# Optimization experiments

Hardware: AMD Instinct MI355X
Metric: run time of the kernel (lower is better)

The kernel has to match this reference:

```python
import jax, jax.numpy as jnp
import numpy as np
from jax import lax

K_SQ = 8  # scaling-and-squaring steps (GridExp default)


def lrelu(x):
    return jnp.where(x >= 0, x, 0.2 * x)


def conv(x, w, b, stride=1):
    y = lax.conv_general_dilated(x, w, (stride,) * 3, 'SAME',
                                 dimension_numbers=('NCDHW', 'OIDHW', 'NCDHW'))
    return y + b[None, :, None, None, None]


def convt(x, w, b):
    y = lax.conv_transpose(x, w, (2, 2, 2), 'SAME',
                           dimension_numbers=('NCDHW', 'OIDHW', 'NCDHW'))
    return y + b[None, :, None, None, None]


def identity_grid(shape):
    rng = [jnp.arange(s, dtype=jnp.float32) for s in shape]
    return jnp.stack(jnp.meshgrid(*rng, indexing='ij'), axis=-1)


def pull_one(img, grid, extrapolate):
    # img (C, X, Y, Z); grid (..., 3) in voxel coordinates; trilinear sampling
    X, Y, Z = img.shape[1:]
    g0f = jnp.floor(grid)
    w = grid - g0f
    g0 = g0f.astype(jnp.int32)
    flat = img.reshape(img.shape[0], -1)
    out = jnp.zeros(img.shape[:1] + grid.shape[:-1], img.dtype)
    for dx in (0, 1):
        for dy in (0, 1):
            for dz in (0, 1):
                ix = jnp.clip(g0[..., 0] + dx, 0, X - 1)
                iy = jnp.clip(g0[..., 1] + dy, 0, Y - 1)
                iz = jnp.clip(g0[..., 2] + dz, 0, Z - 1)
                idx = (ix * Y + iy) * Z + iz
                val = jnp.take(flat, idx.reshape(-1), axis=1).reshape(out.shape)
                wgt = ((w[..., 0] if dx else 1 - w[..., 0]) *
                       (w[..., 1] if dy else 1 - w[..., 1]) *
                       (w[..., 2] if dz else 1 - w[..., 2]))
                out = out + wgt[None] * val
    if not extrapolate:  # zero outside the field of view (GridPull extrapolate=False)
        inb = ((grid[..., 0] >= 0) & (grid[..., 0] <= X - 1) &
               (grid[..., 1] >= 0) & (grid[..., 1] <= Y - 1) &
               (grid[..., 2] >= 0) & (grid[..., 2] <= Z - 1))
        out = out * inb[None]
    return out


pull_batch = jax.vmap(pull_one, in_axes=(0, 0, None))


def resize_field(field, out_shape, value_scale):
    # field (B, X, Y, Z, D) channel-last; trilinear resize (align-centers), scale values
    in_shape = field.shape[1:-1]
    coords = identity_grid(out_shape)
    scale = jnp.array([(i - 1) / (o - 1) for i, o in zip(in_shape, out_shape)], jnp.float32)
    coords = coords * scale
    f = jnp.moveaxis(field, -1, 1)
    cb = jnp.broadcast_to(coords, (field.shape[0],) + coords.shape)
    out = pull_batch(f, cb, True)
    return jnp.moveaxis(out, 1, -1) * value_scale


def affine_basis_cso():
    # CSO in 3D: 3 translations + 3 rotations + 1 isotropic zoom -> 7 params
    B = np.zeros((7, 4, 4), np.float32)
    for i in range(3):
        B[i, i, 3] = 1.0
    for k, (i, j) in enumerate([(0, 1), (0, 2), (1, 2)]):
        B[3 + k, i, j] = 1.0
        B[3 + k, j, i] = -1.0
    for i in range(3):
        B[6, i, i] = 1.0
    return jnp.asarray(B)


def forward_core(source, target, cnn_w, cnn_b, enc_w, enc_b, up_w, up_b, dec_w, dec_b, fin_w, fin_b):
    x = jnp.concatenate([source, target], axis=1)  # (B, 2, X, Y, Z)
    # ---- affine head CNN: 4 strided convs + head conv + global reduction -> (B, 7)
    h = x
    for i in range(4):
        h = lrelu(conv(h, cnn_w[i], cnn_b[i], stride=2))
    h = conv(h, cnn_w[4], cnn_b[4])
    aff_prm = h.mean(axis=(2, 3, 4))
    # ---- UNet velocity head -> (B, X, Y, Z, 3)
    skips = [x]
    h = x
    for i in range(4):
        h = lrelu(conv(h, enc_w[i], enc_b[i], stride=2))
        skips.append(h)
    for i in range(4):
        h = lrelu(convt(h, up_w[i], up_b[i]))
        h = jnp.concatenate([h, skips[3 - i]], axis=1)
        h = lrelu(conv(h, dec_w[i], dec_b[i]))
    vel = jnp.moveaxis(conv(h, fin_w, fin_b), 1, -1)
    shape = vel.shape[1:-1]
    small = tuple(s // 2 for s in shape)
    # ---- exp(): downsample velocity (displacement: values scaled by 0.5)
    v_small = resize_field(vel, small, 0.5)
    idg = identity_grid(small)
    d = v_small / (2.0 ** K_SQ)
    for _ in range(K_SQ):  # scaling and squaring: d <- d + d o (id + d)
        d = d + jnp.moveaxis(pull_batch(jnp.moveaxis(d, -1, 1), idg[None] + d, True), 1, -1)
    grid = resize_field(idg[None] + d, shape, 2.0)  # grid: coords scaled by 2
    # ---- affine exponential, re-centered composition
    basis = affine_basis_cso()
    A = jax.vmap(lambda p: jax.scipy.linalg.expm(jnp.einsum('k,kij->ij', p, basis)))(aff_prm)
    shift = jnp.eye(4, dtype=jnp.float32).at[:3, 3].set(-jnp.asarray(shape, jnp.float32) / 2)
    A = jnp.linalg.solve(shift[None], A @ shift[None])  # inv(shift) @ A @ shift
    lin, off = A[:, :3, :3], A[:, :3, 3]
    grid = jnp.einsum('bij,bxyzj->bxyzi', lin, grid) + off[:, None, None, None, :]
    # ---- warp source
    deformed = pull_batch(source, grid, False)
    return deformed, vel, aff_prm


def setup_inputs() -> dict:
    key = jax.random.key(0)
    ks = iter(jax.random.split(key, 48))

    def p(shape):
        return jax.random.normal(next(ks), shape, jnp.float32) * 0.05

    d = {}
    d['source'] = jax.random.normal(next(ks), (1, 1, 96, 96, 96), jnp.float32)
    d['target'] = jax.random.normal(next(ks), (1, 1, 96, 96, 96), jnp.float32)
    for i, (o, c) in enumerate([(16, 2), (32, 16), (32, 32), (32, 32), (7, 32)]):
        d[f'cnn_w{i}'] = p((o, c, 3, 3, 3)); d[f'cnn_b{i}'] = p((o,))
    for i, (o, c) in enumerate([(16, 2), (32, 16), (32, 32), (32, 32)]):
        d[f'enc_w{i}'] = p((o, c, 3, 3, 3)); d[f'enc_b{i}'] = p((o,))
    for i, (o, c) in enumerate([(32, 32), (32, 32), (32, 32), (16, 32)]):
        d[f'up_w{i}'] = p((o, c, 3, 3, 3)); d[f'up_b{i}'] = p((o,))
    for i, (o, c) in enumerate([(32, 64), (32, 64), (32, 48), (16, 18)]):
        d[f'dec_w{i}'] = p((o, c, 3, 3, 3)); d[f'dec_b{i}'] = p((o,))
    d['fin_w'] = p((3, 16, 3, 3, 3)); d['fin_b'] = p((3,))
    return d


def reference(source, target,
              cnn_w0, cnn_b0, cnn_w1, cnn_b1, cnn_w2, cnn_b2, cnn_w3, cnn_b3, cnn_w4, cnn_b4,
              enc_w0, enc_b0, enc_w1, enc_b1, enc_w2, enc_b2, enc_w3, enc_b3,
              up_w0, up_b0, up_w1, up_b1, up_w2, up_b2, up_w3, up_b3,
              dec_w0, dec_b0, dec_w1, dec_b1, dec_w2, dec_b2, dec_w3, dec_b3,
              fin_w, fin_b):
    return forward_core(
        source, target,
        [cnn_w0, cnn_w1, cnn_w2, cnn_w3, cnn_w4], [cnn_b0, cnn_b1, cnn_b2, cnn_b3, cnn_b4],
        [enc_w0, enc_w1, enc_w2, enc_w3], [enc_b0, enc_b1, enc_b2, enc_b3],
        [up_w0, up_w1, up_w2, up_w3], [up_b0, up_b1, up_b2, up_b3],
        [dec_w0, dec_w1, dec_w2, dec_w3], [dec_b0, dec_b1, dec_b2, dec_b3],
        fin_w, fin_b)
```

## Files before the change

### kernel.cpp

```cpp
#include <hip/hip_runtime.h>

#define N96 884736
#define N48 110592
#define N24 13824
#define N12 1728
#define N6  216

typedef __attribute__((ext_vector_type(4))) short short4v;
typedef __attribute__((ext_vector_type(8))) short short8v;
typedef __attribute__((ext_vector_type(4))) float f32x4;

static __device__ __forceinline__ float lrelu_f(float x){ return x >= 0.f ? x : 0.2f*x; }
static __device__ __forceinline__ int clampi(int v,int lo,int hi){ return v<lo?lo:(v>hi?hi:v); }

static __device__ __forceinline__ short f2bf(float x){
    unsigned u = __builtin_bit_cast(unsigned, x);
    unsigned r = (u + 0x7FFFu + ((u >> 16) & 1u)) >> 16;
    return (short)r;
}

template<int OCPB, int S, bool RELU>
static __device__ __forceinline__ void conv_body(
    const float* __restrict__ in1, int C1,
    const float* __restrict__ in2, int C2,
    const float* __restrict__ w, const float* __restrict__ b,
    float* __restrict__ out, int ID, int OD,
    long out_cstride, int out_vmul, int t, int oc0)
{
    int i2 = t % OD; int r = t / OD; int i1 = r % OD; int i0 = r / OD;

    float acc[OCPB];
    #pragma unroll
    for (int j=0; j<OCPB; ++j) acc[j] = b[oc0+j];

    int zz[3], yy[3], xx[3]; bool zv[3], yv[3], xv[3];
    #pragma unroll
    for (int k=0; k<3; ++k){
        int a0 = (S==2) ? (2*i0+k) : (i0+k-1);
        int a1 = (S==2) ? (2*i1+k) : (i1+k-1);
        int a2 = (S==2) ? (2*i2+k) : (i2+k-1);
        zz[k]=a0; zv[k]=(a0>=0)&&(a0<ID);
        yy[k]=a1; yv[k]=(a1>=0)&&(a1<ID);
        xx[k]=a2; xv[k]=(a2>=0)&&(a2<ID);
    }
    const int C = C1 + C2;
    const int ID2 = ID*ID;
    const long ID3 = (long)ID2*ID;

    for (int s=0; s<2; ++s){
        const float* ip = s ? in2 : in1;
        int Cs  = s ? C2 : C1;
        int icb = s ? C1 : 0;
        if (Cs == 0) continue;
        for (int ic=0; ic<Cs; ++ic){
            const float* ipb = ip + (long)ic*ID3;
            float v[27];
            #pragma unroll
            for (int kd=0; kd<3; ++kd)
            #pragma unroll
            for (int kh=0; kh<3; ++kh)
            #pragma unroll
            for (int kw=0; kw<3; ++kw){
                bool ok = zv[kd] && yv[kh] && xv[kw];
                v[kd*9+kh*3+kw] = ok ? ipb[(long)zz[kd]*ID2 + yy[kh]*ID + xx[kw]] : 0.f;
            }
            const float* wbase = w + ((long)oc0*C + (icb+ic))*27;
            #pragma unroll
            for (int j=0; j<OCPB; ++j){
                const float* wo = wbase + (long)j*C*27;
                float sacc = 0.f;
                #pragma unroll
                for (int k=0; k<27; ++k) sacc += wo[k]*v[k];
                acc[j] += sacc;
            }
        }
    }
    #pragma unroll
    for (int j=0; j<OCPB; ++j){
        float o = RELU ? lrelu_f(acc[j]) : acc[j];
        out[(long)(oc0+j)*out_cstride + (long)t*out_vmul] = o;
    }
}

template<int OCPB, int S, bool RELU>
__global__ void conv3d_k(const float* __restrict__ in1, int C1,
                         const float* __restrict__ in2, int C2,
                         const float* __restrict__ w, const float* __restrict__ b,
                         float* __restrict__ out, int ID, int OD,
                         long out_cstride, int out_vmul)
{
    int nvox = OD*OD*OD;
    int t = blockIdx.x*blockDim.x + threadIdx.x;
    if (t >= nvox) return;
    conv_body<OCPB,S,RELU>(in1,C1,in2,C2,w,b,out,ID,OD,out_cstride,out_vmul,t,blockIdx.y*OCPB);
}

template<int OCPB, int S, bool RELU>
__global__ void conv3d_dual_k(const float* __restrict__ in1A, const float* __restrict__ in2A,
                              const float* __restrict__ in1B, const float* __restrict__ in2B,
                              int C1, int C2,
                              const float* __restrict__ wA, const float* __restrict__ bA,
                              const float* __restrict__ wB, const float* __restrict__ bB,
                              float* __restrict__ outA, float* __restrict__ outB,
                              int ID, int OD)
{
    int nvox = OD*OD*OD;
    int t = blockIdx.x*blockDim.x + threadIdx.x;
    if (t >= nvox) return;
    long nv = nvox;
    if (blockIdx.z == 0)
        conv_body<OCPB,S,RELU>(in1A,C1,in2A,C2,wA,bA,outA,ID,OD,nv,1,t,blockIdx.y*OCPB);
    else
        conv_body<OCPB,S,RELU>(in1B,C1,in2B,C2,wB,bB,outB,ID,OD,nv,1,t,blockIdx.y*OCPB);
}

__global__ void e0cl16_k(const float* __restrict__ e0, short* __restrict__ cl){
    int t = blockIdx.x*blockDim.x + threadIdx.x;
    if (t >= N48) return;
    short8v v0, v1;
    #pragma unroll
    for (int c=0;c<8;++c){ v0[c] = f2bf(e0[(long)c*N48 + t]); v1[c] = f2bf(e0[(long)(8+c)*N48 + t]); }
    *(short8v*)(cl + (long)t*16)     = v0;
    *(short8v*)(cl + (long)t*16 + 8) = v1;
}

__global__ __launch_bounds__(256, 2)
void conv_s2mfma_k(const short* __restrict__ cl,
                   const short* __restrict__ pack,
                   const float* __restrict__ b,
                   float* __restrict__ out)
{
    const short8v zero8 = {0,0,0,0,0,0,0,0};
    int lane = threadIdx.x & 63;
    int nb = gridDim.x;
    int bid = blockIdx.x;
    int sb = (bid & 7)*(nb >> 3) + (bid >> 3);
    int wid = sb*4 + (threadIdx.x >> 6);
    int ot = wid & 1;
    int s  = wid >> 1;
    int l15 = lane & 15, g = lane >> 4;
    int vL = s*16 + l15;
    int xL = vL % 24; int rL = vL/24; int yL = rL % 24; int zL = rL/24;
    const bool gok = (g < 2);

    float bias = b[ot*16 + l15];
    f32x4 acc = {bias,bias,bias,bias};

    #pragma unroll
    for (int kz=0; kz<3; ++kz){
        int iz = 2*zL + kz; bool okz = (iz < 48);
        int izc = okz ? iz : 0;
        #pragma unroll
        for (int ky=0; ky<3; ++ky){
            int iy = 2*yL + ky; bool oky = (iy < 48);
            int iyc = oky ? iy : 0;
            #pragma unroll
            for (int kx=0; kx<3; ++kx){
                int ix = 2*xL + kx; bool okx = (ix < 48);
                int ixc = okx ? ix : 0;
                bool ok = okz && oky && okx && gok;
                long base = (((long)izc*48 + iyc)*48 + ixc)*16 + (gok ? 8*g : 0);
                short8v a = *(const short8v*)(cl + base);
                if (!ok) a = zero8;
                int kidx = kz*9 + ky*3 + kx;
                short8v wfr = *(const short8v*)(pack + (((long)ot*27 + kidx)*64 + lane)*8);
                acc = __builtin_amdgcn_mfma_f32_16x16x32_bf16(a, wfr, acc, 0, 0, 0);
            }
        }
    }

    int oc = ot*16 + l15;
    #pragma unroll
    for (int reg=0; reg<4; ++reg){
        int m = 4*g + reg;
        out[(long)oc*N24 + s*16 + m] = lrelu_f(acc[reg]);
    }
}

__global__ void e3cl_k(const float* __restrict__ e3, short* __restrict__ cl){
    int t = blockIdx.x*blockDim.x + threadIdx.x;
    if (t >= N6) return;
    #pragma unroll
    for (int grp=0; grp<4; ++grp){
        short8v v;
        #pragma unroll
        for (int c=0;c<8;++c) v[c] = f2bf(e3[(long)(8*grp+c)*N6 + t]);
        *(short8v*)(cl + (long)t*32 + 8*grp) = v;
    }
}

__global__ void fill_e0_k(const float* __restrict__ e0, short* __restrict__ cl){
    int t = blockIdx.x*blockDim.x + threadIdx.x;
    if (t >= N48) return;
    short8v v0, v1;
    #pragma unroll
    for (int c=0;c<8;++c)  v0[c] = f2bf(e0[(long)c*N48 + t]);
    #pragma unroll
    for (int c=0;c<8;++c)  v1[c] = f2bf(e0[(long)(8+c)*N48 + t]);
    *(short8v*)(cl + (long)t*48 + 32) = v0;
    *(short8v*)(cl + (long)t*48 + 40) = v1;
}

template<int NV>
__global__ void fill_skip32_k(const float* __restrict__ e, short* __restrict__ cl){
    int t = blockIdx.x*blockDim.x + threadIdx.x;
    if (t >= NV) return;
    #pragma unroll
    for (int grp=0; grp<4; ++grp){
        short8v v;
        #pragma unroll
        for (int c=0;c<8;++c) v[c] = f2bf(e[(long)(8*grp+c)*NV + t]);
        *(short8v*)(cl + (long)t*64 + 32 + 8*grp) = v;
    }
}

static __device__ __forceinline__ void pack_std_d(const float* __restrict__ w, short* __restrict__ pack,
                                                  int t, int CREAL, int OCREAL){
    int kidx = t >> 6, lane = t & 63;
    int oc = lane & 15, g = lane >> 4;
    short8v f;
    #pragma unroll
    for (int j=0;j<8;++j){
        int ic = 8*g + j;
        float val = (oc < OCREAL && ic < CREAL) ? w[((long)oc*CREAL + ic)*27 + kidx] : 0.f;
        f[j] = f2bf(val);
    }
    *(short8v*)(pack + (long)t*8) = f;
}
static __device__ __forceinline__ void pack_2x2_d(const float* __restrict__ w, short* __restrict__ pack,
                                                  int t, int C){
    int lane = t & 63;
    int r = t >> 6;
    int kidx = r % 27;
    int kt = (r/27) & 1;
    int ot = r/54;
    int oc = ot*16 + (lane & 15), g = lane >> 4;
    short8v f;
    #pragma unroll
    for (int j=0;j<8;++j){
        int ic = kt*32 + 8*g + j;
        float val = (ic < C) ? w[((long)oc*C + ic)*27 + kidx] : 0.f;
        f[j] = f2bf(val);
    }
    *(short8v*)(pack + (long)t*8) = f;
}
static __device__ __forceinline__ void pack_up_d(const float* __restrict__ w, short* __restrict__ pack, int t){
    int lane = t & 63;
    int r = t >> 6;
    int kidx = r % 27;
    int ot = r/27;
    int oc = ot*16 + (lane & 15), g = lane >> 4;
    short8v f;
    #pragma unroll
    for (int j=0;j<8;++j){
        int ic = 8*g + j;
        f[j] = f2bf(w[((long)oc*32 + ic)*27 + kidx]);
    }
    *(short8v*)(pack + (long)t*8) = f;
}
static __device__ __forceinline__ void pack_s2_d(const float* __restrict__ w, short* __restrict__ pack, int t){
    int lane = t & 63;
    int r = t >> 6;
    int kidx = r % 27;
    int ot = r/27;
    int oc = ot*16 + (lane & 15), g = lane >> 4;
    short8v f;
    #pragma unroll
    for (int j=0;j<8;++j){
        int ic = 8*g + j;
        float val = (ic < 16) ? w[((long)oc*16 + ic)*27 + kidx] : 0.f;
        f[j] = f2bf(val);
    }
    *(short8v*)(pack + (long)t*8) = f;
}

__global__ void pack_all_k(const float* __restrict__ dw3, const float* __restrict__ fw,
                           const float* __restrict__ uw3,
                           const float* __restrict__ dw2, const float* __restrict__ dw1,
                           const float* __restrict__ dw0,
                           const float* __restrict__ uw2, const float* __restrict__ uw1,
                           const float* __restrict__ uw0,
                           const float* __restrict__ ew1,
                           short* __restrict__ PK3, short* __restrict__ PKF, short* __restrict__ PKU,
                           short* __restrict__ PK2, short* __restrict__ PK1, short* __restrict__ PK0,
                           short* __restrict__ PKU2, short* __restrict__ PKU1, short* __restrict__ PKU0,
                           short* __restrict__ PKE1)
{
    int t = blockIdx.x*blockDim.x + threadIdx.x;
    const int S1 = 27*64;
    const int S4 = 4*27*64;
    const int S2 = 2*27*64;
    if (t < S1){ pack_std_d(dw3, PK3, t, 18, 16); return; } t -= S1;
    if (t < S1){ pack_std_d(fw,  PKF, t, 16,  3); return; } t -= S1;
    if (t < S1){ pack_std_d(uw3, PKU, t, 32, 16); return; } t -= S1;
    if (t < S4){ pack_2x2_d(dw2, PK2, t, 48); return; } t -= S4;
    if (t < S4){ pack_2x2_d(dw1, PK1, t, 64); return; } t -= S4;
    if (t < S4){ pack_2x2_d(dw0, PK0, t, 64); return; } t -= S4;
    if (t < S2){ pack_up_d(uw2, PKU2, t); return; } t -= S2;
    if (t < S2){ pack_up_d(uw1, PKU1, t); return; } t -= S2;
    if (t < S2){ pack_up_d(uw0, PKU0, t); return; } t -= S2;
    if (t < S2){ pack_s2_d(ew1, PKE1, t); return; }
}

template<int CSTR, int OCREAL, bool RELU, int OMODE>
__global__ __launch_bounds__(256, 4)
void conv_mfma2_k(const short* __restrict__ cl,
                  const short* __restrict__ pack,
                  const float* __restrict__ b,
                  void* __restrict__ outp)
{
    const int D2 = 96*96;
    const short8v zero8 = {0,0,0,0,0,0,0,0};
    __shared__ short lwfr[27*64*8];
    for (int idx = threadIdx.x; idx < 27*64; idx += 256)
        *(short8v*)(lwfr + (long)idx*8) = *(const short8v*)(pack + (long)idx*8);
    __syncthreads();

    int lane = threadIdx.x & 63;
    int nb = gridDim.x;
    int bid = blockIdx.x;
    int sb = (bid & 7)*(nb >> 3) + (bid >> 3);
    int wid = sb*4 + (threadIdx.x >> 6);
    int l15 = lane & 15, g = lane >> 4;
    int xh = wid & 1;
    int rem = wid >> 1;
    int y = rem % 96;
    int z = (rem / 96)*2;
    int x0b = xh*48;
    const bool gok = (8*g < CSTR);
    const int go = gok ? 8*g : 0;

    float bias = (l15 < OCREAL) ? b[l15] : 0.f;
    f32x4 acc[2][3];
    #pragma unroll
    for (int o=0;o<2;++o)
    #pragma unroll
    for (int i=0;i<3;++i) acc[o][i] = (f32x4){bias,bias,bias,bias};

    #pragma unroll
    for (int dzr=-1; dzr<=2; ++dzr){
        int zz = z + dzr;
        bool okz = (zz>=0) && (zz<96);
        int zc = okz ? zz : z;
        #pragma unroll
        for (int dy=-1; dy<=1; ++dy){
            int yy = y+dy;
            bool okrow = okz && (yy>=0) && (yy<96);
            int yc = (yy>=0 && yy<96) ? yy : y;
            long rowb = (long)zc*D2 + (long)yc*96;
            #pragma unroll
            for (int dx=-1; dx<=1; ++dx){
                short8v a[3];
                #pragma unroll
                for (int i=0;i<3;++i){
                    int x = x0b + 16*i + l15 + dx;
                    bool okx = (x>=0) && (x<96);
                    int xc = okx ? x : (x0b + 16*i + l15);
                    a[i] = *(const short8v*)(cl + (rowb + xc)*CSTR + go);
                    bool oka = okrow && okx && gok;
                    if (!oka) a[i] = zero8;
                }
                if (dzr >= -1 && dzr <= 1){
                    int kidx = (dzr+1)*9 + (dy+1)*3 + (dx+1);
                    short8v wfr = *(const short8v*)(lwfr + ((long)kidx*64 + lane)*8);
                    #pragma unroll
                    for (int i=0;i<3;++i)
                        acc[0][i] = __builtin_amdgcn_mfma_f32_16x16x32_bf16(a[i], wfr, acc[0][i], 0, 0, 0);
                }
                if (dzr >= 0 && dzr <= 2){
                    int kidx = (dzr)*9 + (dy+1)*3 + (dx+1);
                    short8v wfr = *(const short8v*)(lwfr + ((long)kidx*64 + lane)*8);
                    #pragma unroll
                    for (int i=0;i<3;++i)
                        acc[1][i] = __builtin_amdgcn_mfma_f32_16x16x32_bf16(a[i], wfr, acc[1][i], 0, 0, 0);
                }
            }
        }
    }

    #pragma unroll
    for (int o=0;o<2;++o){
        long vrow = (long)(z+o)*D2 + (long)y*96 + x0b;
        if (OMODE == 0){
            short* op = (short*)outp;
            #pragma unroll
            for (int i=0;i<3;++i)
            #pragma unroll
            for (int reg=0; reg<4; ++reg){
                int mr = 4*g + reg;
                float v = RELU ? lrelu_f(acc[o][i][reg]) : acc[o][i][reg];
                op[(vrow + 16*i + mr)*16 + l15] = f2bf(v);
            }
        } else {
            float* op = (float*)outp;
            if (l15 < 3){
                #pragma unroll
                for (int i=0;i<3;++i)
                #pragma unroll
                for (int reg=0; reg<4; ++reg){
                    int mr = 4*g + reg;
                    op[(vrow + 16*i + mr)*3 + l15] = acc[o][i][reg];
                }
            }
        }
    }
}

__global__ __launch_bounds__(256, 2)
void conv_mfma48_k(const short* __restrict__ cl,
                   const short* __restrict__ pack,
                   const float* __restrict__ b,
                   short* __restrict__ out)
{
    const int D2 = 48*48;
    const short8v zero8 = {0,0,0,0,0,0,0,0};
    int lane = threadIdx.x & 63;
    int nb = gridDim.x;
    int bid = blockIdx.x;
    int sb = (bid & 7)*(nb >> 3) + (bid >> 3);
    int wid = sb*4 + (threadIdx.x >> 6);
    int l15 = lane & 15, g = lane >> 4;
    int y = wid % 48, z = wid / 48;
    const bool g1ok = (g < 2);
    const int go1 = g1ok ? (32 + 8*g) : 0;

    float bias0 = b[l15];
    float bias1 = b[16 + l15];
    f32x4 acc[2][3];
    #pragma unroll
    for (int i=0;i<3;++i){ acc[0][i] = (f32x4){bias0,bias0,bias0,bias0};
                           acc[1][i] = (f32x4){bias1,bias1,bias1,bias1}; }

    #pragma unroll
    for (int dz=-1; dz<=1; ++dz){
        int zz = z+dz;
        bool okz = (zz>=0) && (zz<48);
        int zc = okz ? zz : z;
        #pragma unroll
        for (int dy=-1; dy<=1; ++dy){
            int yy = y+dy;
            bool okzy = okz && (yy>=0) && (yy<48);
            int yc = (yy>=0 && yy<48) ? yy : y;
            long rowb = (long)zc*D2 + (long)yc*48;
            #pragma unroll
            for (int dx=-1; dx<=1; ++dx){
                int kidx = (dz+1)*9 + (dy+1)*3 + (dx+1);
                short8v a0[3], a1[3];
                #pragma unroll
                for (int i=0;i<3;++i){
                    int x = 16*i + l15 + dx;
                    bool okx = (x>=0) && (x<48);
                    int xc = okx ? x : (16*i + l15);
                    bool ok = okzy && okx;
                    long base = (rowb + xc)*48;
                    a0[i] = *(const short8v*)(cl + base + 8*g);
                    a1[i] = *(const short8v*)(cl + base + go1);
                    if (!ok) a0[i] = zero8;
                    if (!(ok && g1ok)) a1[i] = zero8;
                }
                #pragma unroll
                for (int ot=0; ot<2; ++ot){
                    short8v wfr0 = *(const short8v*)(pack + (((long)(ot*2+0)*27 + kidx)*64 + lane)*8);
                    short8v wfr1 = *(const short8v*)(pack + (((long)(ot*2+1)*27 + kidx)*64 + lane)*8);
                    #pragma unroll
                    for (int i=0;i<3;++i){
                        acc[ot][i] = __builtin_amdgcn_mfma_f32_16x16x32_bf16(a0[i], wfr0, acc[ot][i], 0, 0, 0);
                        acc[ot][i] = __builtin_amdgcn_mfma_f32_16x16x32_bf16(a1[i], wfr1, acc[ot][i], 0, 0, 0);
                    }
                }
            }
        }
    }

    long vrow = (long)z*D2 + (long)y*48;
    #pragma unroll
    for (int ot=0; ot<2; ++ot)
    #pragma unroll
    for (int i=0;i<3;++i)
    #pragma unroll
    for (int reg=0; reg<4; ++reg){
        int mr = 4*g + reg;
        out[(vrow + 16*i + mr)*32 + ot*16 + l15] = f2bf(lrelu_f(acc[ot][i][reg]));
    }
}

template<int D>
__global__ __launch_bounds__(256, 2)
void conv_mfmaD_k(const short* __restrict__ cl,
                  const short* __restrict__ pack,
                  const float* __restrict__ b,
                  short* __restrict__ out)
{
    const short8v zero8 = {0,0,0,0,0,0,0,0};
    int lane = threadIdx.x & 63;
    int nb = gridDim.x;
    int bid = blockIdx.x;
    int sb = ((nb & 7) == 0) ? ((bid & 7)*(nb >> 3) + (bid >> 3)) : bid;
    int wid = sb*4 + (threadIdx.x >> 6);
    int ot = wid & 1;
    int s  = wid >> 1;
    int l15 = lane & 15, g = lane >> 4;
    int vL = s*16 + l15;
    int xL = vL % D; int rL = vL/D; int yL = rL % D; int zL = rL/D;

    float bias = b[ot*16 + l15];
    f32x4 acc = {bias,bias,bias,bias};

    #pragma unroll
    for (int dz=-1; dz<=1; ++dz){
        int iz = zL+dz; bool okz = (iz>=0)&&(iz<D); int izc = okz?iz:zL;
        #pragma unroll
        for (int dy=-1; dy<=1; ++dy){
            int iy = yL+dy; bool oky = (iy>=0)&&(iy<D); int iyc = oky?iy:yL;
            #pragma unroll
            for (int dx=-1; dx<=1; ++dx){
                int ix = xL+dx; bool okx = (ix>=0)&&(ix<D); int ixc = okx?ix:xL;
                bool ok = okz && oky && okx;
                long base = (((long)izc*D + iyc)*D + ixc)*64;
                int kidx = (dz+1)*9 + (dy+1)*3 + (dx+1);
                #pragma unroll
                for (int kt=0; kt<2; ++kt){
                    short8v wfr = *(const short8v*)(pack + (((long)(ot*2+kt)*27 + kidx)*64 + lane)*8);
                    short8v a = *(const short8v*)(cl + base + kt*32 + 8*g);
                    if (!ok) a = zero8;
                    acc = __builtin_amdgcn_mfma_f32_16x16x32_bf16(a, wfr, acc, 0, 0, 0);
                }
            }
        }
    }

    #pragma unroll
    for (int reg=0; reg<4; ++reg){
        int m = 4*g + reg;
        out[(long)(s*16 + m)*32 + ot*16 + l15] = f2bf(lrelu_f(acc[reg]));
    }
}

template<int IDI, int NST, int OSTR>
__global__ __launch_bounds__(256, 2)
void convt_mfmaup_k(const short* __restrict__ cl,
                    const short* __restrict__ pack,
                    const float* __restrict__ b,
                    short* __restrict__ o)
{
    const int D2i = IDI*IDI;
    const int OD = 2*IDI;
    const long D2o = (long)OD*OD;
    int lane = threadIdx.x & 63;
    int nb = gridDim.x;
    int bid = blockIdx.x;
    int sb = ((nb & 7) == 0) ? ((bid & 7)*(nb >> 3) + (bid >> 3)) : bid;
    int wid = sb*4 + (threadIdx.x >> 6);
    int px = wid & 1;
    int row = wid >> 1;
    int y = row % OD, z = row / OD;
    int l15 = lane & 15, g = lane >> 4;
    int pz = z & 1, py = y & 1, hz = z >> 1, hy = y >> 1;

    float bias0 = b[l15], bias1 = b[16 + l15];
    f32x4 acc[2][NST];
    #pragma unroll
    for (int i=0;i<NST;++i){ acc[0][i] = (f32x4){bias0,bias0,bias0,bias0};
                             acc[1][i] = (f32x4){bias1,bias1,bias1,bias1}; }

    int k0s[2], izs[2], nz=0;
    if (pz){ k0s[0]=1; izs[0]=hz; nz=1; }
    else { if (hz>=1){ k0s[nz]=0; izs[nz]=hz-1; ++nz; } k0s[nz]=2; izs[nz]=hz; ++nz; }
    int k1s[2], iys[2], ny=0;
    if (py){ k1s[0]=1; iys[0]=hy; ny=1; }
    else { if (hy>=1){ k1s[ny]=0; iys[ny]=hy-1; ++ny; } k1s[ny]=2; iys[ny]=hy; ++ny; }

    for (int a=0;a<nz;++a)
    for (int c=0;c<ny;++c){
        long rowb = (long)izs[a]*D2i + (long)iys[c]*IDI;
        int kbase = k0s[a]*9 + k1s[c]*3;
        int nqx = px?1:2;
        for (int qx=0; qx<nqx; ++qx){
            int k2 = px ? 1 : 2*qx;
            int xoff = px ? 0 : (qx-1);
            short8v av[NST];
            #pragma unroll
            for (int i=0;i<NST;++i){
                int ix = 16*i + l15 + xoff;
                av[i] = (short8v){0,0,0,0,0,0,0,0};
                if (ix >= 0 && ix < IDI) av[i] = *(const short8v*)(cl + ((rowb + ix)*32 + 8*g));
            }
            #pragma unroll
            for (int ot=0; ot<2; ++ot){
                short8v wfr = *(const short8v*)(pack + (((long)ot*27 + kbase + k2)*64 + lane)*8);
                #pragma unroll
                for (int i=0;i<NST;++i)
                    acc[ot][i] = __builtin_amdgcn_mfma_f32_16x16x32_bf16(av[i], wfr, acc[ot][i], 0, 0, 0);
            }
        }
    }

    #pragma unroll
    for (int ot=0; ot<2; ++ot)
    #pragma unroll
    for (int i=0;i<NST;++i)
    #pragma unroll
    for (int reg=0; reg<4; ++reg){
        int m = 16*i + 4*g + reg;
        if (m < IDI){
            long vox = (long)z*D2o + (long)y*OD + (2*m + px);
            o[vox*OSTR + ot*16 + l15] = f2bf(lrelu_f(acc[ot][i][reg]));
        }
    }
}

__global__ __launch_bounds__(256, 2)
void convt_mfma96_k(const short* __restrict__ cl,
                    const short* __restrict__ pack,
                    const float* __restrict__ b,
                    const float* __restrict__ src,
                    const float* __restrict__ tgt,
                    short* __restrict__ o)
{
    const int D2i = 48*48;
    const long D2o = 96*96;
    int lane = threadIdx.x & 63;
    int nb = gridDim.x;
    int bid = blockIdx.x;
    int sb = (bid & 7)*(nb >> 3) + (bid >> 3);
    int wid = sb*4 + (threadIdx.x >> 6);
    int px = wid & 1;
    int row = wid >> 1;
    int y = row % 96, z = row / 96;
    int l15 = lane & 15, g = lane >> 4;
    int pz = z & 1, py = y & 1, hz = z >> 1, hy = y >> 1;

    float bias = b[l15];
    f32x4 acc[3];
    #pragma unroll
    for (int i=0;i<3;++i) acc[i] = (f32x4){bias,bias,bias,bias};

    int k0s[2], izs[2], nz=0;
    if (pz){ k0s[0]=1; izs[0]=hz; nz=1; }
    else { if (hz>=1){ k0s[nz]=0; izs[nz]=hz-1; ++nz; } k0s[nz]=2; izs[nz]=hz; ++nz; }
    int k1s[2], iys[2], ny=0;
    if (py){ k1s[0]=1; iys[0]=hy; ny=1; }
    else { if (hy>=1){ k1s[ny]=0; iys[ny]=hy-1; ++ny; } k1s[ny]=2; iys[ny]=hy; ++ny; }

    for (int a=0;a<nz;++a)
    for (int c=0;c<ny;++c){
        long rowb = (long)izs[a]*D2i + (long)iys[c]*48;
        int kbase = k0s[a]*9 + k1s[c]*3;
        int nqx = px?1:2;
        for (int qx=0; qx<nqx; ++qx){
            int k2 = px ? 1 : 2*qx;
            int xoff = px ? 0 : (qx-1);
            short8v wfr = *(const short8v*)(pack + ((long)(kbase+k2)*64 + lane)*8);
            #pragma unroll
            for (int i=0;i<3;++i){
                int ix = 16*i + l15 + xoff;
                short8v av = {0,0,0,0,0,0,0,0};
                if (ix >= 0) av = *(const short8v*)(cl + ((rowb + ix)*32 + 8*g));
                acc[i] = __builtin_amdgcn_mfma_f32_16x16x32_bf16(av, wfr, acc[i], 0, 0, 0);
            }
        }
    }

    #pragma unroll
    for (int i=0;i<3;++i)
    #pragma unroll
    for (int reg=0; reg<4; ++reg){
        int m = 16*i + 4*g + reg;
        long vox = (long)z*D2o + (long)y*96 + (2*m + px);
        o[vox*24 + l15] = f2bf(lrelu_f(acc[i][reg]));
        if (l15 == 0)      o[vox*24 + 16] = f2bf(src[vox]);
        else if (l15 == 1) o[vox*24 + 17] = f2bf(tgt[vox]);
        else if (l15 < 8)  o[vox*24 + 16 + l15] = 0;
    }
}

static __device__ void mat4mul(const double* A, const double* B, double* C){
    for (int i=0;i<4;++i) for (int j=0;j<4;++j){
        double s=0; for (int k=0;k<4;++k) s += A[i*4+k]*B[k*4+j];
        C[i*4+j]=s;
    }
}

__global__ void affine_k(const float* __restrict__ c4, float* __restrict__ aff_out, float* __restrict__ mats){
    __shared__ float p[7];
    int t = threadIdx.x;
    if (t < 7){
        float s = 0.f;
        for (int i=0;i<N6;++i) s += c4[t*N6 + i];
        p[t] = s / (float)N6;
        aff_out[t] = p[t];
    }
    __syncthreads();
    if (t == 0){
        double M[16];
        for (int i=0;i<16;++i) M[i]=0.0;
        M[0*4+3]=p[0]; M[1*4+3]=p[1]; M[2*4+3]=p[2];
        M[0*4+1]= p[3]; M[1*4+0]=-p[3];
        M[0*4+2]= p[4]; M[2*4+0]=-p[4];
        M[1*4+2]= p[5]; M[2*4+1]=-p[5];
        M[0*4+0]+=p[6]; M[1*4+1]+=p[6]; M[2*4+2]+=p[6];
        double nrm=0.0;
        for (int i=0;i<4;++i){
            double s=0; for (int j=0;j<4;++j) s += fabs(M[i*4+j]);
            if (s>nrm) nrm=s;
        }
        int jj=0;
        while (nrm > 0.25 && jj < 40){ nrm *= 0.5; ++jj; }
        double sc = 1.0; for (int q=0;q<jj;++q) sc *= 0.5;
        double Ms[16]; for (int i=0;i<16;++i) Ms[i]=M[i]*sc;
        double E[16], T[16], Tn[16];
        for (int i=0;i<16;++i){ E[i] = (i%5==0)?1.0:0.0; T[i]=E[i]; }
        for (int k=1;k<=18;++k){
            mat4mul(T, Ms, Tn);
            double inv = 1.0/(double)k;
            for (int i=0;i<16;++i){ T[i]=Tn[i]*inv; E[i]+=T[i]; }
        }
        for (int q=0;q<jj;++q){ mat4mul(E,E,Tn); for (int i=0;i<16;++i) E[i]=Tn[i]; }
        const double tsh = -48.0;
        for (int i=0;i<3;++i){
            for (int j=0;j<3;++j) mats[i*3+j] = (float)E[i*4+j];
            double rs = (E[i*4+0] - (i==0?1.0:0.0))
                      + (E[i*4+1] - (i==1?1.0:0.0))
                      + (E[i*4+2] - (i==2?1.0:0.0));
            mats[9+i] = (float)(E[i*4+3] + rs*tsh);
        }
    }
}

static __device__ __forceinline__ void trilerp3(const float* __restrict__ f, int D,
                                                float c0, float c1, float c2, float out3[3]){
    float f0=floorf(c0), f1=floorf(c1), f2=floorf(c2);
    float w0=c0-f0, w1=c1-f1, w2=c2-f2;
    int a0=(int)f0, a1=(int)f1, a2=(int)f2;
    int i0s[2]={clampi(a0,0,D-1), clampi(a0+1,0,D-1)};
    int i1s[2]={clampi(a1,0,D-1), clampi(a1+1,0,D-1)};
    int i2s[2]={clampi(a2,0,D-1), clampi(a2+1,0,D-1)};
    float w0s[2]={1.f-w0,w0}, w1s[2]={1.f-w1,w1}, w2s[2]={1.f-w2,w2};
    out3[0]=out3[1]=out3[2]=0.f;
    #pragma unroll
    for (int dx=0;dx<2;++dx)
    #pragma unroll
    for (int dy=0;dy<2;++dy)
    #pragma unroll
    for (int dz=0;dz<2;++dz){
        float wg = w0s[dx]*w1s[dy]*w2s[dz];
        const float* pp = f + ((i0s[dx]*D + i1s[dy])*D + i2s[dz])*3;
        out3[0]+=wg*pp[0]; out3[1]+=wg*pp[1]; out3[2]+=wg*pp[2];
    }
}

static __device__ __forceinline__ float trilerp1(const float* __restrict__ f, int D,
                                                 float c0, float c1, float c2){
    float f0=floorf(c0), f1=floorf(c1), f2=floorf(c2);
    float w0=c0-f0, w1=c1-f1, w2=c2-f2;
    int a0=(int)f0, a1=(int)f1, a2=(int)f2;
    int i0s[2]={clampi(a0,0,D-1), clampi(a0+1,0,D-1)};
    int i1s[2]={clampi(a1,0,D-1), clampi(a1+1,0,D-1)};
    int i2s[2]={clampi(a2,0,D-1), clampi(a2+1,0,D-1)};
    float w0s[2]={1.f-w0,w0}, w1s[2]={1.f-w1,w1}, w2s[2]={1.f-w2,w2};
    float s=0.f;
    #pragma unroll
    for (int dx=0;dx<2;++dx)
    #pragma unroll
    for (int dy=0;dy<2;++dy)
    #pragma unroll
    for (int dz=0;dz<2;++dz){
        float wg = w0s[dx]*w1s[dy]*w2s[dz];
        s += wg * f[(i0s[dx]*D + i1s[dy])*D + i2s[dz]];
    }
    return s;
}

__global__ void resize_small_k(const float* __restrict__ vel, float* __restrict__ dA){
    int t = blockIdx.x*blockDim.x + threadIdx.x;
    if (t >= N48) return;
    int i2 = t % 48; int r = t / 48; int i1 = r % 48; int i0 = r / 48;
    const float s = 95.f/47.f;
    float o[3];
    trilerp3(vel, 96, i0*s, i1*s, i2*s, o);
    const float k = 0.5f/256.f;
    dA[t*3+0]=o[0]*k; dA[t*3+1]=o[1]*k; dA[t*3+2]=o[2]*k;
}

__global__ void sq_k(const float* __restrict__ din, float* __restrict__ dout){
    int t = blockIdx.x*blockDim.x + threadIdx.x;
    if (t >= N48) return;
    int i2 = t % 48; int r = t / 48; int i1 = r % 48; int i0 = r / 48;
    float d0=din[t*3+0], d1=din[t*3+1], d2=din[t*3+2];
    float s[3];
    trilerp3(din, 48, (float)i0+d0, (float)i1+d1, (float)i2+d2, s);
    dout[t*3+0]=d0+s[0]; dout[t*3+1]=d1+s[1]; dout[t*3+2]=d2+s[2];
}

__global__ void grid_pull_k(const float* __restrict__ dfin, const float* __restrict__ src,
                            const float* __restrict__ mats, float* __restrict__ out){
    int t = blockIdx.x*blockDim.x + threadIdx.x;
    if (t >= N96) return;
    int i2 = t % 96; int r = t / 96; int i1 = r % 96; int i0 = r / 96;
    const float sc = 47.f/95.f;
    float c0=i0*sc, c1=i1*sc, c2=i2*sc;
    float s[3];
    trilerp3(dfin, 48, c0, c1, c2, s);
    float g0 = 2.f*(c0+s[0]), g1 = 2.f*(c1+s[1]), g2 = 2.f*(c2+s[2]);
    float L00=mats[0],L01=mats[1],L02=mats[2],L10=mats[3],L11=mats[4],L12=mats[5],
          L20=mats[6],L21=mats[7],L22=mats[8],o0=mats[9],o1=mats[10],o2=mats[11];
    float gg0 = L00*g0 + L01*g1 + L02*g2 + o0;
    float gg1 = L10*g0 + L11*g1 + L12*g2 + o1;
    float gg2 = L20*g0 + L21*g1 + L22*g2 + o2;
    bool inb = (gg0>=0.f)&&(gg0<=95.f)&&(gg1>=0.f)&&(gg1<=95.f)&&(gg2>=0.f)&&(gg2<=95.f);
    float val = trilerp1(src, 96, gg0, gg1, gg2);
    out[t] = inb ? val : 0.f;
}

extern "C" void kernel_launch(void* const* d_in, const int* in_sizes, int n_in,
                              void* d_out, int out_size, void* d_ws, size_t ws_size,
                              hipStream_t stream) {
    const float* src = (const float*)d_in[0];
    const float* tgt = (const float*)d_in[1];
    const float *cw[5], *cb[5], *ew[4], *eb[4], *uw[4], *ub[4], *dw[4], *db[4];
    for (int i=0;i<5;++i){ cw[i]=(const float*)d_in[2+2*i]; cb[i]=(const float*)d_in[3+2*i]; }
    for (int i=0;i<4;++i){ ew[i]=(const float*)d_in[12+2*i]; eb[i]=(const float*)d_in[13+2*i]; }
    for (int i=0;i<4;++i){ uw[i]=(const float*)d_in[20+2*i]; ub[i]=(const float*)d_in[21+2*i]; }
    for (int i=0;i<4;++i){ dw[i]=(const float*)d_in[28+2*i]; db[i]=(const float*)d_in[29+2*i]; }
    const float* fw = (const float*)d_in[36];
    const float* fb = (const float*)d_in[37];

    float* ws = (float*)d_ws;
    const long OFF_E0 = 0;
    const long OFF_CLE0 = OFF_E0 + 16L*N48;
    const long OFF_E1 = OFF_CLE0 + 8L*N48;
    const long OFF_E2 = OFF_E1 + 32L*N24;
    const long OFF_E3 = OFF_E2 + 32L*N12;
    const long OFF_B1 = OFF_E3 + 32L*N6;
    const long OFF_B2 = OFF_B1 + 32L*N48;
    const long OFF_CL24 = OFF_B2 + 32L*N48;
    const long OFF_CL16 = OFF_CL24 + 12L*N96;
    const long OFF_DA = OFF_CL16 + 8L*N96;
    const long OFF_DB = OFF_DA + 3L*N48;
    const long OFF_MT = OFF_DB + 3L*N48;
    const long OFF_PK3 = OFF_MT + 16;
    const long OFF_PKF = OFF_PK3 + 6912;
    const long OFF_PK2 = OFF_PKF + 6912;
    const long OFF_PKU = OFF_PK2 + 27648;
    const long OFF_PK1 = OFF_PKU + 6912;
    const long OFF_PK0 = OFF_PK1 + 27648;
    const long OFF_PKU2 = OFF_PK0 + 27648;
    const long OFF_PKU1 = OFF_PKU2 + 13824;
    const long OFF_PKU0 = OFF_PKU1 + 13824;
    const long OFF_PKE1 = OFF_PKU0 + 13824;
    const long OFF_CLD2 = OFF_PKE1 + 13824;
    const long OFF_CL64B = OFF_CLD2 + 16L*N48;
    const long OFF_CLD1 = OFF_CL64B + 32L*N24;
    const long OFF_CL64C = OFF_CLD1 + 16L*N24;
    const long OFF_CLD0 = OFF_CL64C + 32L*N12;
    const long OFF_CLE3 = OFF_CLD0 + 16L*N12;
    const long WS_TOT = OFF_CLE3 + 16L*N6;
    if (ws_size < (size_t)WS_TOT*4) return;

    float* E0 = ws + OFF_E0;
    short* CLE0 = (short*)(ws + OFF_CLE0);
    float* E1 = ws + OFF_E1;
    float* E2 = ws + OFF_E2;
    float* E3 = ws + OFF_E3;
    float* B1 = ws + OFF_B1;
    float* B2 = ws + OFF_B2;
    short* CL24 = (short*)(ws + OFF_CL24);
    short* CL16 = (short*)(ws + OFF_CL16);
    short* CL48 = (short*)(ws + OFF_CL16);
    float* DA = ws + OFF_DA;
    float* DB = ws + OFF_DB;
    float* MT = ws + OFF_MT;
    short* PK3 = (short*)(ws + OFF_PK3);
    short* PKF = (short*)(ws + OFF_PKF);
    short* PK2 = (short*)(ws + OFF_PK2);
    short* PKU = (short*)(ws + OFF_PKU);
    short* PK1 = (short*)(ws + OFF_PK1);
    short* PK0 = (short*)(ws + OFF_PK0);
    short* PKU2 = (short*)(ws + OFF_PKU2);
    short* PKU1 = (short*)(ws + OFF_PKU1);
    short* PKU0 = (short*)(ws + OFF_PKU0);
    short* PKE1 = (short*)(ws + OFF_PKE1);
    short* CLD2 = (short*)(ws + OFF_CLD2);
    short* CL64B = (short*)(ws + OFF_CL64B);
    short* CLD1 = (short*)(ws + OFF_CLD1);
    short* CL64C = (short*)(ws + OFF_CL64C);
    short* CLD0 = (short*)(ws + OFF_CLD0);
    short* CLE3 = (short*)(ws + OFF_CLE3);

    float* out_def = (float*)d_out;
    float* out_vel = out_def + N96;
    float* out_aff = out_vel + 3L*N96;

    auto gsz = [](int n, int b){ return (n + b - 1)/b; };

    pack_all_k<<<gsz(39744,256), 256, 0, stream>>>(dw[3], fw, uw[3], dw[2], dw[1], dw[0],
                                                   uw[2], uw[1], uw[0], ew[1],
                                                   PK3, PKF, PKU, PK2, PK1, PK0,
                                                   PKU2, PKU1, PKU0, PKE1);

    conv3d_dual_k< 8,2,true><<<dim3(gsz(N48,256), 2,2), 256, 0, stream>>>(src,tgt, src,tgt, 1,1, cw[0],cb[0], ew[0],eb[0], B1,E0, 96,48);

    e0cl16_k<<<gsz(N48,256), 256, 0, stream>>>(E0, CLE0);

    conv3d_k< 4,2,true><<<dim3(gsz(N24,256), 8), 256, 0, stream>>>(B1,16, nullptr,0, cw[1],cb[1], B2, 48,24, N24, 1);
    conv_s2mfma_k<<<432, 256, 0, stream>>>(CLE0, PKE1, eb[1], E1);

    conv3d_dual_k< 2,2,true><<<dim3(gsz(N12, 64),16,2),  64, 0, stream>>>(B2,nullptr, E1,nullptr, 32,0, cw[2],cb[2], ew[2],eb[2], B1,E2, 24,12);
    conv3d_dual_k< 1,2,true><<<dim3(gsz(N6 , 64),32,2),  64, 0, stream>>>(B1,nullptr, E2,nullptr, 32,0, cw[3],cb[3], ew[3],eb[3], B2,E3, 12, 6);
    conv3d_k< 1,1,false><<<dim3(gsz(N6 , 64), 7), 64, 0, stream>>>(B2,32, nullptr, 0, cw[4], cb[4], B1, 6, 6, N6, 1);
    affine_k<<<1, 64, 0, stream>>>(B1, out_aff, MT);

    e3cl_k<<<1, 256, 0, stream>>>(E3, CLE3);

    convt_mfmaup_k<6,1,64><<<72, 256, 0, stream>>>(CLE3, PKU0, ub[0], CL64C);
    fill_skip32_k<N12><<<gsz(N12,256), 256, 0, stream>>>(E2, CL64C);

    conv_mfmaD_k<12><<<54, 256, 0, stream>>>(CL64C, PK0, db[0], CLD0);

    convt_mfmaup_k<12,1,64><<<288, 256, 0, stream>>>(CLD0, PKU1, ub[1], CL64B);
    fill_skip32_k<N24><<<gsz(N24,256), 256, 0, stream>>>(E1, CL64B);

    conv_mfmaD_k<24><<<432, 256, 0, stream>>>(CL64B, PK1, db[1], CLD1);

    convt_mfmaup_k<24,2,48><<<1152, 256, 0, stream>>>(CLD1, PKU2, ub[2], CL48);
    fill_e0_k<<<gsz(N48,256), 256, 0, stream>>>(E0, CL48);

    conv_mfma48_k<<<576, 256, 0, stream>>>(CL48, PK2, db[2], CLD2);

    convt_mfma96_k<<<4608, 256, 0, stream>>>(CLD2, PKU, ub[3], src, tgt, CL24);

    conv_mfma2_k<24,16,true ,0><<<2304, 256, 0, stream>>>(CL24, PK3, db[3], (void*)CL16);
    conv_mfma2_k<16, 3,false,1><<<2304, 256, 0, stream>>>(CL16, PKF, fb, (void*)out_vel);

    resize_small_k<<<gsz(N48,256), 256, 0, stream>>>(out_vel, DA);
    float* da = DA; float* dbuf = DB;
    for (int it=0; it<8; ++it){
        sq_k<<<gsz(N48,256), 256, 0, stream>>>(da, dbuf);
        float* tmp = da; da = dbuf; dbuf = tmp;
    }

    grid_pull_k<<<gsz(N96,256), 256, 0, stream>>>(da, src, MT, out_def);
}
```

Measured before the change: 465.8 us.

## Compute 2x2 z-y output block per wave in full-res conv kernels

Each wave in the 96^3 MFMA conv kernel now produces a 2x2 block of output rows in z and y instead of two rows in z. Every loaded input row fragment is reused across up to four output rows, so global loads per output drop. Grid size is halved to match. The cost is more accumulator and fragment registers (12 accumulators plus 9 input fragments), which may lower occupancy or cause spills.

```diff
diff --git a/kernel.cpp b/kernel.cpp
--- a/kernel.cpp
+++ b/kernel.cpp
@@ -324,63 +324,71 @@
     int l15 = lane & 15, g = lane >> 4;
     int xh = wid & 1;
     int rem = wid >> 1;
-    int y = rem % 96;
-    int z = (rem / 96)*2;
+    int y = (rem % 48)*2;
+    int z = (rem / 48)*2;
     int x0b = xh*48;
     const bool gok = (8*g < CSTR);
     const int go = gok ? 8*g : 0;
 
     float bias = (l15 < OCREAL) ? b[l15] : 0.f;
-    f32x4 acc[2][3];
-    #pragma unroll
-    for (int o=0;o<2;++o)
-    #pragma unroll
-    for (int i=0;i<3;++i) acc[o][i] = (f32x4){bias,bias,bias,bias};
-
-    #pragma unroll
-    for (int dzr=-1; dzr<=2; ++dzr){
-        int zz = z + dzr;
+    f32x4 acc[2][2][3];
+    #pragma unroll
+    for (int oz=0;oz<2;++oz)
+    #pragma unroll
+    for (int oy=0;oy<2;++oy)
+    #pragma unroll
+    for (int i=0;i<3;++i) acc[oz][oy][i] = (f32x4){bias,bias,bias,bias};
+
+    #pragma unroll
+    for (int zzr=0; zzr<4; ++zzr){
+        int zz = z + zzr - 1;
         bool okz = (zz>=0) && (zz<96);
         int zc = okz ? zz : z;
         #pragma unroll
-        for (int dy=-1; dy<=1; ++dy){
-            int yy = y+dy;
+        for (int yyr=0; yyr<4; ++yyr){
+            int yy = y + yyr - 1;
             bool okrow = okz && (yy>=0) && (yy<96);
             int yc = (yy>=0 && yy<96) ? yy : y;
             long rowb = (long)zc*D2 + (long)yc*96;
-            #pragma unroll
-            for (int dx=-1; dx<=1; ++dx){
-                short8v a[3];
+            short8v a[9];
+            #pragma unroll
+            for (int dxi=0; dxi<3; ++dxi){
                 #pragma unroll
                 for (int i=0;i<3;++i){
-                    int x = x0b + 16*i + l15 + dx;
+                    int x = x0b + 16*i + l15 + dxi - 1;
                     bool okx = (x>=0) && (x<96);
                     int xc = okx ? x : (x0b + 16*i + l15);
-                    a[i] = *(const short8v*)(cl + (rowb + xc)*CSTR + go);
+                    short8v t = *(const short8v*)(cl + (rowb + xc)*CSTR + go);
                     bool oka = okrow && okx && gok;
-                    if (!oka) a[i] = zero8;
+                    a[dxi*3+i] = oka ? t : zero8;
                 }
-                if (dzr >= -1 && dzr <= 1){
-                    int kidx = (dzr+1)*9 + (dy+1)*3 + (dx+1);
-                    short8v wfr = *(const short8v*)(lwfr + ((long)kidx*64 + lane)*8);
+            }
+            #pragma unroll
+            for (int oz=0; oz<2; ++oz){
+                const int dz = zzr - 1 - oz;
+                if (dz < -1 || dz > 1) continue;
+                #pragma unroll
+                for (int oy=0; oy<2; ++oy){
+                    const int dy = yyr - 1 - oy;
+                    if (dy < -1 || dy > 1) continue;
                     #pragma unroll
-                    for (int i=0;i<3;++i)
-                        acc[0][i] = __builtin_amdgcn_mfma_f32_16x16x32_bf16(a[i], wfr, acc[0][i], 0, 0, 0);
+                    for (int dxi=0; dxi<3; ++dxi){
+                        int kidx = (dz+1)*9 + (dy+1)*3 + dxi;
+                        short8v wfr = *(const short8v*)(lwfr + ((long)kidx*64 + lane)*8);
+                        #pragma unroll
+                        for (int i=0;i<3;++i)
+                            acc[oz][oy][i] = __builtin_amdgcn_mfma_f32_16x16x32_bf16(a[dxi*3+i], wfr, acc[oz][oy][i], 0, 0, 0);
+                    }
                 }
-                if (dzr >= 0 && dzr <= 2){
-                    int kidx = (dzr)*9 + (dy+1)*3 + (dx+1);
-                    short8v wfr = *(const short8v*)(lwfr + ((long)kidx*64 + lane)*8);
-                    #pragma unroll
-                    for (int i=0;i<3;++i)
-                        acc[1][i] = __builtin_amdgcn_mfma_f32_16x16x32_bf16(a[i], wfr, acc[1][i], 0, 0, 0);
-                }
-            }
-        }
-    }
-
-    #pragma unroll
-    for (int o=0;o<2;++o){
-        long vrow = (long)(z+o)*D2 + (long)y*96 + x0b;
+            }
+        }
+    }
+
+    #pragma unroll
+    for (int oz=0;oz<2;++oz)
+    #pragma unroll
+    for (int oy=0;oy<2;++oy){
+        long vrow = (long)(z+oz)*D2 + (long)(y+oy)*96 + x0b;
         if (OMODE == 0){
             short* op = (short*)outp;
             #pragma unroll
@@ -388,7 +396,7 @@
             #pragma unroll
             for (int reg=0; reg<4; ++reg){
                 int mr = 4*g + reg;
-                float v = RELU ? lrelu_f(acc[o][i][reg]) : acc[o][i][reg];
+                float v = RELU ? lrelu_f(acc[oz][oy][i][reg]) : acc[oz][oy][i][reg];
                 op[(vrow + 16*i + mr)*16 + l15] = f2bf(v);
             }
         } else {
@@ -399,7 +407,7 @@
                 #pragma unroll
                 for (int reg=0; reg<4; ++reg){
                     int mr = 4*g + reg;
-                    op[(vrow + 16*i + mr)*3 + l15] = acc[o][i][reg];
+                    op[(vrow + 16*i + mr)*3 + l15] = acc[oz][oy][i][reg];
                 }
             }
         }
@@ -929,8 +937,8 @@
 
     convt_mfma96_k<<<4608, 256, 0, stream>>>(CLD2, PKU, ub[3], src, tgt, CL24);
 
-    conv_mfma2_k<24,16,true ,0><<<2304, 256, 0, stream>>>(CL24, PK3, db[3], (void*)CL16);
-    conv_mfma2_k<16, 3,false,1><<<2304, 256, 0, stream>>>(CL16, PKF, fb, (void*)out_vel);
+    conv_mfma2_k<24,16,true ,0><<<1152, 256, 0, stream>>>(CL24, PK3, db[3], (void*)CL16);
+    conv_mfma2_k<16, 3,false,1><<<1152, 256, 0, stream>>>(CL16, PKF, fb, (void*)out_vel);
 
     resize_small_k<<<gsz(N48,256), 256, 0, stream>>>(out_vel, DA);
     float* da = DA; float* dbuf = DB;
```

Result: slower. 846.0 us (+81.6%).
